# Optimization experiments

Hardware: AMD Instinct MI355X
Metric: run time of the kernel (lower is better)

Reference implementation:

```python
import jax, jax.numpy as jnp
import numpy as np

N_E = 1024
E_DIM = 64
BETA = 0.25
DECAY = 0.99
EPSILON = 1e-5


def setup_inputs() -> dict:
    key = jax.random.key(0)
    k1, k2, k3 = jax.random.split(key, 3)
    z = jax.random.normal(k1, (32, E_DIM, 32, 32), dtype=jnp.float32)
    # codebook initialized uniform(-1/n_e, 1/n_e) as in the torch module
    emb_w = jax.random.uniform(k2, (N_E, E_DIM), minval=-1.0 / N_E, maxval=1.0 / N_E, dtype=jnp.float32)
    ema_cluster_size = jnp.ones((N_E,), dtype=jnp.float32)
    ema_w = jax.random.uniform(k3, (N_E, E_DIM), minval=-1.0 / N_E, maxval=1.0 / N_E, dtype=jnp.float32)
    return {"z": z, "emb_w": emb_w, "ema_cluster_size": ema_cluster_size, "ema_w": ema_w}


def reference(z, emb_w, ema_cluster_size, ema_w):
    B, C, H, W = z.shape  # C == E_DIM
    zf = jnp.transpose(z, (0, 2, 3, 1)).reshape(-1, E_DIM)  # [N, e_dim]
    N = zf.shape[0]

    # squared-distance via ||z||^2 + ||e||^2 - 2 z.e (same expansion as torch code)
    d = (jnp.sum(zf * zf, axis=1, keepdims=True)
         + jnp.sum(emb_w * emb_w, axis=1)
         - 2.0 * zf @ emb_w.T)  # [N, n_e]
    idx = jnp.argmin(d, axis=1)  # [N]

    min_encodings = jax.nn.one_hot(idx, N_E, dtype=jnp.float32)  # [N, n_e]
    # cluster stats via scatter-add (equivalent to one-hot matmuls, cheaper)
    cluster_size = jax.ops.segment_sum(jnp.ones((N,), jnp.float32), idx, num_segments=N_E)
    sum_encodings = jax.ops.segment_sum(zf, idx, num_segments=N_E)  # [n_e, e_dim]

    # EMA update (training path, done before the z_q lookup as in torch)
    new_cs = DECAY * ema_cluster_size + (1.0 - DECAY) * cluster_size
    new_w = DECAY * ema_w + (1.0 - DECAY) * sum_encodings
    n = jnp.sum(new_cs)
    cs_norm = (new_cs + EPSILON) / (n + N_E * EPSILON) * n
    new_emb = new_w / cs_norm[:, None]  # updated codebook

    z_q = new_emb[idx].reshape(B, H, W, C).transpose(0, 3, 1, 2)  # [B,C,H,W]
    loss = BETA * jnp.mean((jax.lax.stop_gradient(z_q) - z) ** 2)
    z_q_st = z + jax.lax.stop_gradient(z_q - z)  # straight-through

    avg_probs = cluster_size / N
    perplexity = jnp.exp(-jnp.sum(avg_probs * jnp.log(avg_probs + 1e-10)))
    return loss, z_q_st, perplexity, min_encodings, idx
```

## Files before the change

kernel.cpp:

```cpp
#include <hip/hip_runtime.h>
#include <math.h>

#define NVEC 32768
#define NE   1024
#define ED   64
#define TOT  2097152
#define NCHUNK 4
#define CHUNK  256
#define MT     128

#define O_LOSS   0
#define O_ZQ     1
#define O_PERP   2097153
#define O_MINENC 2097154
#define O_IDX    35651586

#define W_PIDX   0
#define W_CS     32768
#define W_SUMENC 33792
#define W_ESQ    164864


__global__ void __launch_bounds__(256) k_pre(const float* __restrict__ emb,
                                             float* __restrict__ ws,
                                             float* __restrict__ out) {
    int b = blockIdx.x;
    if (b < 65) {
        int i = b * 256 + threadIdx.x;
        float4 zv; zv.x = 0.f; zv.y = 0.f; zv.z = 0.f; zv.w = 0.f;
        *(float4*)(ws + W_CS + i * 4) = zv;
        if (b == 0 && threadIdx.x == 0) out[O_LOSS] = 0.f;
    } else {
        int code = (b - 65) * 256 + threadIdx.x;
        const float* ep = emb + (size_t)code * ED;
        float r[8];
#pragma unroll
        for (int j = 0; j < 8; ++j) r[j] = __fmul_rn(ep[j], ep[j]);
#pragma unroll
        for (int i = 8; i < 64; i += 8)
#pragma unroll
            for (int j = 0; j < 8; ++j)
                r[j] = __fadd_rn(r[j], __fmul_rn(ep[i + j], ep[i + j]));
        ws[W_ESQ + code] = __fadd_rn(
            __fadd_rn(__fadd_rn(r[0], r[1]), __fadd_rn(r[2], r[3])),
            __fadd_rn(__fadd_rn(r[4], r[5]), __fadd_rn(r[6], r[7])));
    }
}

__device__ __forceinline__ int apos(int m) {
    return ((m & 4) << 4) + ((m >> 3) << 2) + (m & 3);
}

__global__ void __launch_bounds__(512) k_dist(const float* __restrict__ z,
                                              const float* __restrict__ emb,
                                              const float* __restrict__ esq_g,
                                              int* __restrict__ fidx,
                                              int* __restrict__ cnt,
                                              float* __restrict__ sumenc,
                                              float* __restrict__ out) {
    __shared__ __align__(16) float s_a[64 * 128];
    __shared__ __align__(16) float s_b[2 * 64 * 132];
    __shared__ float s_esq[CHUNK];
    __shared__ float s_zsq[MT];
    __shared__ int s_bi[MT];

    int tid = threadIdx.x;
    int n0 = blockIdx.x * MT;
    int b = n0 >> 10, hw0 = n0 & 1023;
    const float* zb = z + b * 65536 + hw0;

#pragma unroll
    for (int j = 0; j < 4; ++j) {
        int f4i = j * 512 + tid;
        int q = f4i & 31, c = f4i >> 5;
        float4 v = *(const float4*)(zb + (c << 10) + q * 4);
        v.x = __fmul_rn(2.0f, v.x);
        v.y = __fmul_rn(2.0f, v.y);
        v.z = __fmul_rn(2.0f, v.z);
        v.w = __fmul_rn(2.0f, v.w);
        *(float4*)(s_a + c * 128 + ((q & 1) << 6) + ((q >> 1) << 2)) = v;
    }
    __syncthreads();

    if (tid < MT) {
        int p = apos(tid);
        float r[8];
#pragma unroll
        for (int j = 0; j < 8; ++j) {
            float v = s_a[j * 128 + p];
            r[j] = __fmul_rn(v, v);
        }
#pragma unroll
        for (int i = 8; i < 64; i += 8)
#pragma unroll
            for (int j = 0; j < 8; ++j) {
                float v = s_a[(i + j) * 128 + p];
                r[j] = __fadd_rn(r[j], __fmul_rn(v, v));
            }
        s_zsq[tid] = __fmul_rn(0.25f, __fadd_rn(
            __fadd_rn(__fadd_rn(r[0], r[1]), __fadd_rn(r[2], r[3])),
            __fadd_rn(__fadd_rn(r[4], r[5]), __fadd_rn(r[6], r[7]))));
    }
    __syncthreads();

    int mi = tid & 15, ki = tid >> 4;
    int kbase = ki * 8;
    int kk = ki & 15;
    const float* sbk = s_b + (ki >> 4) * 8448;
    float zs[8];
#pragma unroll
    for (int mu = 0; mu < 8; ++mu) zs[mu] = s_zsq[8 * mi + mu];

    float bd[8];
    int bix[8];
#pragma unroll
    for (int mu = 0; mu < 8; ++mu) { bd[mu] = 3.4e38f; bix[mu] = kbase; }

    for (int ch = 0; ch < NCHUNK; ++ch) {
        int k0 = ch * CHUNK;
        __syncthreads();
#pragma unroll
        for (int j = 0; j < 8; ++j) {
            int f4i = j * 512 + tid;
            int kl = f4i >> 4, c4 = f4i & 15;
            float4 v = *(const float4*)(emb + (size_t)(k0 + kl) * ED + c4 * 4);
            int sc = kl >> 7, klr = kl & 127;
            float* sb = s_b + sc * 8448;
            int base = (((klr >> 2) + c4) & 31) * 4 + (klr & 3);
            sb[(c4 * 4 + 0) * 132 + base] = v.x;
            sb[(c4 * 4 + 1) * 132 + base] = v.y;
            sb[(c4 * 4 + 2) * 132 + base] = v.z;
            sb[(c4 * 4 + 3) * 132 + base] = v.w;
        }
        if (tid < CHUNK) s_esq[tid] = esq_g[k0 + tid];
        __syncthreads();

        float acc[8][8];
#pragma unroll
        for (int mu = 0; mu < 8; ++mu)
#pragma unroll
            for (int ku = 0; ku < 8; ++ku) acc[mu][ku] = 0.f;

        for (int cg = 0; cg < 64; cg += 4) {
            float4 A0[4], A1[4], B0[4], B1[4];
#pragma unroll
            for (int j = 0; j < 4; ++j) {
                int c = cg + j;
                int c4 = c >> 2;
                const float* ar = s_a + c * 128 + (mi << 2);
                A0[j] = *(const float4*)(ar);
                A1[j] = *(const float4*)(ar + 64);
                B0[j] = *(const float4*)(sbk + c * 132 + ((2 * kk + c4) & 31) * 4);
                B1[j] = *(const float4*)(sbk + c * 132 + ((2 * kk + 1 + c4) & 31) * 4);
            }
#pragma unroll
            for (int j = 0; j < 4; ++j) {
#pragma unroll
                for (int mu = 0; mu < 8; ++mu) {
                    float a = (mu < 4) ? (&A0[j].x)[mu] : (&A1[j].x)[mu - 4];
                    acc[mu][0] = __fmaf_rn(a, B0[j].x, acc[mu][0]);
                    acc[mu][1] = __fmaf_rn(a, B0[j].y, acc[mu][1]);
                    acc[mu][2] = __fmaf_rn(a, B0[j].z, acc[mu][2]);
                    acc[mu][3] = __fmaf_rn(a, B0[j].w, acc[mu][3]);
                    acc[mu][4] = __fmaf_rn(a, B1[j].x, acc[mu][4]);
                    acc[mu][5] = __fmaf_rn(a, B1[j].y, acc[mu][5]);
                    acc[mu][6] = __fmaf_rn(a, B1[j].z, acc[mu][6]);
                    acc[mu][7] = __fmaf_rn(a, B1[j].w, acc[mu][7]);
                }
            }
        }

#pragma unroll
        for (int mu = 0; mu < 8; ++mu)
#pragma unroll
            for (int ku = 0; ku < 8; ++ku) {
                float d = __fsub_rn(__fadd_rn(zs[mu], s_esq[kbase + ku]),
                                    acc[mu][ku]);
                if (d < bd[mu]) { bd[mu] = d; bix[mu] = k0 + kbase + ku; }
            }
    }

    __syncthreads();
    float* red_d = s_b;
    int* red_i = (int*)(s_b + 4096);
#pragma unroll
    for (int mu = 0; mu < 8; ++mu) {
        red_d[ki * 128 + 8 * mi + mu] = bd[mu];
        red_i[ki * 128 + 8 * mi + mu] = bix[mu];
    }
    __syncthreads();
    if (tid < MT) {
        float best = red_d[tid];
        int bi = red_i[tid];
#pragma unroll
        for (int q = 1; q < 32; ++q) {
            float d = red_d[q * 128 + tid];
            int i = red_i[q * 128 + tid];
            if (d < best || (d == best && i < bi)) { best = d; bi = i; }
        }
        fidx[n0 + tid] = bi;
        out[O_IDX + n0 + tid] = (float)bi;
        s_bi[tid] = bi;
        atomicAdd(&cnt[bi], 1);
    }
    __syncthreads();

    {
        int m = tid & 127, qt = tid >> 7;
        int p = apos(m);
#pragma unroll
        for (int j = 0; j < 16; ++j) {
            int c = qt * 16 + j;
            s_b[m * 65 + c] = __fmul_rn(0.5f, s_a[c * 128 + p]);
        }
    }
    __syncthreads();

    {
        int lane = tid & 63, w = tid >> 6;
#pragma unroll
        for (int t = 0; t < 16; ++t) {
            int m = (w << 4) | t;
            int bi = s_bi[m];
            float v = s_b[m * 65 + lane];
            unsafeAtomicAdd(sumenc + ((size_t)bi << 6) + lane, v);
        }
    }
}

__global__ void __launch_bounds__(256) k_zq(const float* __restrict__ z,
                                            const int* __restrict__ idx,
                                            const float* __restrict__ ema_cs,
                                            const float* __restrict__ ema_w,
                                            const int* __restrict__ cnt,
                                            const float* __restrict__ sumenc,
                                            float* __restrict__ out) {
    __shared__ float s_csn[NE];
    __shared__ float swn[4], swe[4];
    __shared__ int sbi[16];
    int tid = threadIdx.x;
    bool doent = (blockIdx.x == 0);

    float myncs[4];
    float rn = 0.f, re = 0.f;
#pragma unroll
    for (int j = 0; j < 4; ++j) {
        int k = j * 256 + tid;
        float c = (float)cnt[k];
        float ncs = 0.99f * ema_cs[k] + (1.0f - 0.99f) * c;
        myncs[j] = ncs;
        rn += ncs;
        if (doent) {
            float p = c * (1.0f / (float)NVEC);
            re += p * logf(p + 1e-10f);
        }
    }
#pragma unroll
    for (int o = 32; o > 0; o >>= 1) {
        rn += __shfl_down(rn, o, 64);
        re += __shfl_down(re, o, 64);
    }
    int wave = tid >> 6;
    if ((tid & 63) == 0) { swn[wave] = rn; swe[wave] = re; }
    if (tid < 16) sbi[tid] = idx[blockIdx.x * 16 + tid];
    __syncthreads();
    float nt = (swn[0] + swn[1]) + (swn[2] + swn[3]);
    if (doent && tid == 0) {
        float te = (swe[0] + swe[1]) + (swe[2] + swe[3]);
        out[O_PERP] = expf(-te);
    }
#pragma unroll
    for (int j = 0; j < 4; ++j) {
        int k = j * 256 + tid;
        s_csn[k] = (myncs[j] + 1e-5f) / (nt + 1024.0f * 1e-5f) * nt;
    }
    __syncthreads();

    float local = 0.f;
#pragma unroll
    for (int i = 0; i < 4; ++i) {
        int t = blockIdx.x * 256 + tid + i * 524288;
        int b = t >> 16, c = (t >> 10) & 63, hw = t & 1023;
        int n = (b << 10) | hw;
        int g = idx[n] * ED + c;
        float nw = 0.99f * ema_w[g] + (1.0f - 0.99f) * sumenc[g];
        float e = nw / s_csn[g >> 6];
        float zv = z[t];
        float diff = e - zv;
        out[O_ZQ + t] = zv + diff;
        local = fmaf(diff, diff, local);
    }

    int t = tid;
    int r0 = blockIdx.x * 16;
    for (int r = 0; r < 16; ++r) {
        int rbi = sbi[r];
        float* rp = out + O_MINENC + (size_t)(r0 + r) * NE;
        if (t < 254) {
            int col = 2 + t * 4;
            float4 v;
            v.x = (col == rbi) ? 1.0f : 0.0f;
            v.y = (col + 1 == rbi) ? 1.0f : 0.0f;
            v.z = (col + 2 == rbi) ? 1.0f : 0.0f;
            v.w = (col + 3 == rbi) ? 1.0f : 0.0f;
            *(float4*)(rp + col) = v;
        } else if (t == 254) {
            float2 v;
            v.x = (0 == rbi) ? 1.0f : 0.0f;
            v.y = (1 == rbi) ? 1.0f : 0.0f;
            *(float2*)(rp) = v;
        } else {
            float4 v;
            v.x = (1018 == rbi) ? 1.0f : 0.0f;
            v.y = (1019 == rbi) ? 1.0f : 0.0f;
            v.z = (1020 == rbi) ? 1.0f : 0.0f;
            v.w = (1021 == rbi) ? 1.0f : 0.0f;
            *(float4*)(rp + 1018) = v;
            float2 w;
            w.x = (1022 == rbi) ? 1.0f : 0.0f;
            w.y = (1023 == rbi) ? 1.0f : 0.0f;
            *(float2*)(rp + 1022) = w;
        }
    }

#pragma unroll
    for (int o = 32; o > 0; o >>= 1) local += __shfl_down(local, o, 64);
    __shared__ float sp[4];
    if ((tid & 63) == 0) sp[wave] = local;
    __syncthreads();
    if (tid == 0)
        unsafeAtomicAdd(out + O_LOSS,
                        ((sp[0] + sp[1]) + (sp[2] + sp[3])) * (0.25f / (float)TOT));
}

extern "C" void kernel_launch(void* const* d_in, const int* in_sizes, int n_in,
                              void* d_out, int out_size, void* d_ws, size_t ws_size,
                              hipStream_t stream) {
    const float* z      = (const float*)d_in[0];
    const float* emb    = (const float*)d_in[1];
    const float* ema_cs = (const float*)d_in[2];
    const float* ema_w  = (const float*)d_in[3];
    float* out = (float*)d_out;
    float* ws  = (float*)d_ws;

    k_pre<<<69, 256, 0, stream>>>(emb, ws, out);
    k_dist<<<NVEC / MT, 512, 0, stream>>>(z, emb, ws + W_ESQ, (int*)(ws + W_PIDX),
                                          (int*)(ws + W_CS), ws + W_SUMENC, out);
    k_zq<<<2048, 256, 0, stream>>>(z, (const int*)(ws + W_PIDX), ema_cs, ema_w,
                                   (const int*)(ws + W_CS), ws + W_SUMENC, out);
}
```

Baseline: 244.3 us.

## Read codebook directly from global/L1 instead of staging chunks in LDS

The distance kernel no longer copies 256-code chunks of the codebook into shared memory with block-wide barriers. Each thread now loads its own 8 codebook rows straight from global memory (through cache) as float4s, and all 1024 squared norms are preloaded once. This removes the per-chunk LDS transpose stores and syncs and shrinks shared memory use, which may raise occupancy. In exchange, codebook reads become per-thread strided global loads that rely on L1/L2 hit rates, and lanes in a wavefront read overlapping rows.

```diff
diff --git a/kernel.cpp b/kernel.cpp
--- a/kernel.cpp
+++ b/kernel.cpp
@@ -5,9 +5,7 @@
 #define NE   1024
 #define ED   64
 #define TOT  2097152
-#define NCHUNK 4
-#define CHUNK  256
-#define MT     128
+#define MT   128
 
 #define O_LOSS   0
 #define O_ZQ     1
@@ -59,8 +57,8 @@
                                               float* __restrict__ sumenc,
                                               float* __restrict__ out) {
     __shared__ __align__(16) float s_a[64 * 128];
-    __shared__ __align__(16) float s_b[2 * 64 * 132];
-    __shared__ float s_esq[CHUNK];
+    __shared__ __align__(16) float s_scr[8448];
+    __shared__ float s_esq[NE];
     __shared__ float s_zsq[MT];
     __shared__ int s_bi[MT];
 
@@ -80,6 +78,8 @@
         v.w = __fmul_rn(2.0f, v.w);
         *(float4*)(s_a + c * 128 + ((q & 1) << 6) + ((q >> 1) << 2)) = v;
     }
+    s_esq[tid] = esq_g[tid];
+    s_esq[tid + 512] = esq_g[tid + 512];
     __syncthreads();
 
     if (tid < MT) {
@@ -104,9 +104,7 @@
     __syncthreads();
 
     int mi = tid & 15, ki = tid >> 4;
-    int kbase = ki * 8;
-    int kk = ki & 15;
-    const float* sbk = s_b + (ki >> 4) * 8448;
+    int kb8 = ki * 8;
     float zs[8];
 #pragma unroll
     for (int mu = 0; mu < 8; ++mu) zs[mu] = s_zsq[8 * mi + mu];
@@ -114,26 +112,11 @@
     float bd[8];
     int bix[8];
 #pragma unroll
-    for (int mu = 0; mu < 8; ++mu) { bd[mu] = 3.4e38f; bix[mu] = kbase; }
-
-    for (int ch = 0; ch < NCHUNK; ++ch) {
-        int k0 = ch * CHUNK;
-        __syncthreads();
-#pragma unroll
-        for (int j = 0; j < 8; ++j) {
-            int f4i = j * 512 + tid;
-            int kl = f4i >> 4, c4 = f4i & 15;
-            float4 v = *(const float4*)(emb + (size_t)(k0 + kl) * ED + c4 * 4);
-            int sc = kl >> 7, klr = kl & 127;
-            float* sb = s_b + sc * 8448;
-            int base = (((klr >> 2) + c4) & 31) * 4 + (klr & 3);
-            sb[(c4 * 4 + 0) * 132 + base] = v.x;
-            sb[(c4 * 4 + 1) * 132 + base] = v.y;
-            sb[(c4 * 4 + 2) * 132 + base] = v.z;
-            sb[(c4 * 4 + 3) * 132 + base] = v.w;
-        }
-        if (tid < CHUNK) s_esq[tid] = esq_g[k0 + tid];
-        __syncthreads();
+    for (int mu = 0; mu < 8; ++mu) { bd[mu] = 3.4e38f; bix[mu] = kb8; }
+
+    for (int ch = 0; ch < 4; ++ch) {
+        int k0 = ch * 256;
+        const float* eb = emb + (size_t)(k0 + kb8) * ED;
 
         float acc[8][8];
 #pragma unroll
@@ -141,31 +124,24 @@
 #pragma unroll
             for (int ku = 0; ku < 8; ++ku) acc[mu][ku] = 0.f;
 
-        for (int cg = 0; cg < 64; cg += 4) {
-            float4 A0[4], A1[4], B0[4], B1[4];
+#pragma unroll 4
+        for (int c4 = 0; c4 < 16; ++c4) {
+            float4 B[8];
+#pragma unroll
+            for (int ku = 0; ku < 8; ++ku)
+                B[ku] = *(const float4*)(eb + ku * ED + c4 * 4);
 #pragma unroll
             for (int j = 0; j < 4; ++j) {
-                int c = cg + j;
-                int c4 = c >> 2;
+                int c = c4 * 4 + j;
                 const float* ar = s_a + c * 128 + (mi << 2);
-                A0[j] = *(const float4*)(ar);
-                A1[j] = *(const float4*)(ar + 64);
-                B0[j] = *(const float4*)(sbk + c * 132 + ((2 * kk + c4) & 31) * 4);
-                B1[j] = *(const float4*)(sbk + c * 132 + ((2 * kk + 1 + c4) & 31) * 4);
-            }
-#pragma unroll
-            for (int j = 0; j < 4; ++j) {
+                float4 a0 = *(const float4*)(ar);
+                float4 a1 = *(const float4*)(ar + 64);
 #pragma unroll
                 for (int mu = 0; mu < 8; ++mu) {
-                    float a = (mu < 4) ? (&A0[j].x)[mu] : (&A1[j].x)[mu - 4];
-                    acc[mu][0] = __fmaf_rn(a, B0[j].x, acc[mu][0]);
-                    acc[mu][1] = __fmaf_rn(a, B0[j].y, acc[mu][1]);
-                    acc[mu][2] = __fmaf_rn(a, B0[j].z, acc[mu][2]);
-                    acc[mu][3] = __fmaf_rn(a, B0[j].w, acc[mu][3]);
-                    acc[mu][4] = __fmaf_rn(a, B1[j].x, acc[mu][4]);
-                    acc[mu][5] = __fmaf_rn(a, B1[j].y, acc[mu][5]);
-                    acc[mu][6] = __fmaf_rn(a, B1[j].z, acc[mu][6]);
-                    acc[mu][7] = __fmaf_rn(a, B1[j].w, acc[mu][7]);
+                    float a = (mu < 4) ? (&a0.x)[mu] : (&a1.x)[mu - 4];
+#pragma unroll
+                    for (int ku = 0; ku < 8; ++ku)
+                        acc[mu][ku] = __fmaf_rn(a, (&B[ku].x)[j], acc[mu][ku]);
                 }
             }
         }
@@ -174,15 +150,14 @@
         for (int mu = 0; mu < 8; ++mu)
 #pragma unroll
             for (int ku = 0; ku < 8; ++ku) {
-                float d = __fsub_rn(__fadd_rn(zs[mu], s_esq[kbase + ku]),
+                float d = __fsub_rn(__fadd_rn(zs[mu], s_esq[k0 + kb8 + ku]),
                                     acc[mu][ku]);
-                if (d < bd[mu]) { bd[mu] = d; bix[mu] = k0 + kbase + ku; }
+                if (d < bd[mu]) { bd[mu] = d; bix[mu] = k0 + kb8 + ku; }
             }
     }
 
-    __syncthreads();
-    float* red_d = s_b;
-    int* red_i = (int*)(s_b + 4096);
+    float* red_d = s_scr;
+    int* red_i = (int*)(s_scr + 4096);
 #pragma unroll
     for (int mu = 0; mu < 8; ++mu) {
         red_d[ki * 128 + 8 * mi + mu] = bd[mu];
@@ -211,7 +186,7 @@
 #pragma unroll
         for (int j = 0; j < 16; ++j) {
             int c = qt * 16 + j;
-            s_b[m * 65 + c] = __fmul_rn(0.5f, s_a[c * 128 + p]);
+            s_scr[m * 65 + c] = __fmul_rn(0.5f, s_a[c * 128 + p]);
         }
     }
     __syncthreads();
@@ -222,7 +197,7 @@
         for (int t = 0; t < 16; ++t) {
             int m = (w << 4) | t;
             int bi = s_bi[m];
-            float v = s_b[m * 65 + lane];
+            float v = s_scr[m * 65 + lane];
             unsafeAtomicAdd(sumenc + ((size_t)bi << 6) + lane, v);
         }
     }
```

New measurement: 250.7 us. 2.6% more time.

## Split codebook search across two blocks per tile and add merge kernel

Applied to the files above, without the earlier changes.

The distance kernel now launches two 256-thread blocks per 128-vector tile. Each block scans half the codebook and writes its partial best distance and index into scratch space in the min_encodings output region. A new merge kernel picks the winner, writes the indices and counts, and does the sum-of-encodings atomics by reading z directly. The aim is more blocks and smaller LDS use per block, for better occupancy. The cost is an extra kernel launch and extra global traffic, and the scratch use of the output buffer relies on k_zq overwriting min_encodings later.

```diff
diff --git a/kernel.cpp b/kernel.cpp
--- a/kernel.cpp
+++ b/kernel.cpp
@@ -6,7 +6,7 @@
 #define ED   64
 #define TOT  2097152
 #define NCHUNK 4
-#define CHUNK  256
+#define CHUNK  128
 #define MT     128
 
 #define O_LOSS   0
@@ -51,27 +51,24 @@
     return ((m & 4) << 4) + ((m >> 3) << 2) + (m & 3);
 }
 
-__global__ void __launch_bounds__(512) k_dist(const float* __restrict__ z,
+__global__ void __launch_bounds__(256) k_dist(const float* __restrict__ z,
                                               const float* __restrict__ emb,
                                               const float* __restrict__ esq_g,
-                                              int* __restrict__ fidx,
-                                              int* __restrict__ cnt,
-                                              float* __restrict__ sumenc,
                                               float* __restrict__ out) {
     __shared__ __align__(16) float s_a[64 * 128];
-    __shared__ __align__(16) float s_b[2 * 64 * 132];
+    __shared__ __align__(16) float s_b[64 * 132];
     __shared__ float s_esq[CHUNK];
     __shared__ float s_zsq[MT];
-    __shared__ int s_bi[MT];
 
     int tid = threadIdx.x;
-    int n0 = blockIdx.x * MT;
+    int tile = blockIdx.x >> 1, khalf = blockIdx.x & 1;
+    int n0 = tile * MT;
     int b = n0 >> 10, hw0 = n0 & 1023;
     const float* zb = z + b * 65536 + hw0;
 
 #pragma unroll
-    for (int j = 0; j < 4; ++j) {
-        int f4i = j * 512 + tid;
+    for (int j = 0; j < 8; ++j) {
+        int f4i = j * 256 + tid;
         int q = f4i & 31, c = f4i >> 5;
         float4 v = *(const float4*)(zb + (c << 10) + q * 4);
         v.x = __fmul_rn(2.0f, v.x);
@@ -105,8 +102,6 @@
 
     int mi = tid & 15, ki = tid >> 4;
     int kbase = ki * 8;
-    int kk = ki & 15;
-    const float* sbk = s_b + (ki >> 4) * 8448;
     float zs[8];
 #pragma unroll
     for (int mu = 0; mu < 8; ++mu) zs[mu] = s_zsq[8 * mi + mu];
@@ -114,23 +109,21 @@
     float bd[8];
     int bix[8];
 #pragma unroll
-    for (int mu = 0; mu < 8; ++mu) { bd[mu] = 3.4e38f; bix[mu] = kbase; }
+    for (int mu = 0; mu < 8; ++mu) { bd[mu] = 3.4e38f; bix[mu] = khalf * 512 + kbase; }
 
     for (int ch = 0; ch < NCHUNK; ++ch) {
-        int k0 = ch * CHUNK;
+        int k0 = khalf * 512 + ch * CHUNK;
         __syncthreads();
 #pragma unroll
         for (int j = 0; j < 8; ++j) {
-            int f4i = j * 512 + tid;
+            int f4i = j * 256 + tid;
             int kl = f4i >> 4, c4 = f4i & 15;
             float4 v = *(const float4*)(emb + (size_t)(k0 + kl) * ED + c4 * 4);
-            int sc = kl >> 7, klr = kl & 127;
-            float* sb = s_b + sc * 8448;
-            int base = (((klr >> 2) + c4) & 31) * 4 + (klr & 3);
-            sb[(c4 * 4 + 0) * 132 + base] = v.x;
-            sb[(c4 * 4 + 1) * 132 + base] = v.y;
-            sb[(c4 * 4 + 2) * 132 + base] = v.z;
-            sb[(c4 * 4 + 3) * 132 + base] = v.w;
+            int base = (((kl >> 2) + c4) & 31) * 4 + (kl & 3);
+            s_b[(c4 * 4 + 0) * 132 + base] = v.x;
+            s_b[(c4 * 4 + 1) * 132 + base] = v.y;
+            s_b[(c4 * 4 + 2) * 132 + base] = v.z;
+            s_b[(c4 * 4 + 3) * 132 + base] = v.w;
         }
         if (tid < CHUNK) s_esq[tid] = esq_g[k0 + tid];
         __syncthreads();
@@ -150,8 +143,8 @@
                 const float* ar = s_a + c * 128 + (mi << 2);
                 A0[j] = *(const float4*)(ar);
                 A1[j] = *(const float4*)(ar + 64);
-                B0[j] = *(const float4*)(sbk + c * 132 + ((2 * kk + c4) & 31) * 4);
-                B1[j] = *(const float4*)(sbk + c * 132 + ((2 * kk + 1 + c4) & 31) * 4);
+                B0[j] = *(const float4*)(s_b + c * 132 + ((2 * ki + c4) & 31) * 4);
+                B1[j] = *(const float4*)(s_b + c * 132 + ((2 * ki + 1 + c4) & 31) * 4);
             }
 #pragma unroll
             for (int j = 0; j < 4; ++j) {
@@ -182,7 +175,7 @@
 
     __syncthreads();
     float* red_d = s_b;
-    int* red_i = (int*)(s_b + 4096);
+    int* red_i = (int*)(s_b + 2048);
 #pragma unroll
     for (int mu = 0; mu < 8; ++mu) {
         red_d[ki * 128 + 8 * mi + mu] = bd[mu];
@@ -193,37 +186,54 @@
         float best = red_d[tid];
         int bi = red_i[tid];
 #pragma unroll
-        for (int q = 1; q < 32; ++q) {
+        for (int q = 1; q < 16; ++q) {
             float d = red_d[q * 128 + tid];
             int i = red_i[q * 128 + tid];
             if (d < best || (d == best && i < bi)) { best = d; bi = i; }
         }
-        fidx[n0 + tid] = bi;
-        out[O_IDX + n0 + tid] = (float)bi;
+        out[O_MINENC + khalf * 32768 + n0 + tid] = best;
+        ((int*)(out + O_MINENC))[65536 + khalf * 32768 + n0 + tid] = bi;
+    }
+}
+
+__global__ void __launch_bounds__(256) k_mrg(const float* __restrict__ z,
+                                             int* __restrict__ fidx,
+                                             int* __restrict__ cnt,
+                                             float* __restrict__ sumenc,
+                                             float* __restrict__ out) {
+    __shared__ int s_bi[MT];
+    int tid = threadIdx.x;
+    int m0 = blockIdx.x * MT;
+
+    if (tid < MT) {
+        int m = m0 + tid;
+        const float* cd = out + O_MINENC;
+        const int* ci = (const int*)(out + O_MINENC) + 65536;
+        float d0 = cd[m], d1 = cd[32768 + m];
+        int i0 = ci[m], i1 = ci[32768 + m];
+        int bi = (d1 < d0) ? i1 : i0;
+        fidx[m] = bi;
+        out[O_IDX + m] = (float)bi;
         s_bi[tid] = bi;
         atomicAdd(&cnt[bi], 1);
     }
     __syncthreads();
 
-    {
-        int m = tid & 127, qt = tid >> 7;
-        int p = apos(m);
-#pragma unroll
-        for (int j = 0; j < 16; ++j) {
-            int c = qt * 16 + j;
-            s_b[m * 65 + c] = __fmul_rn(0.5f, s_a[c * 128 + p]);
-        }
-    }
-    __syncthreads();
-
-    {
-        int lane = tid & 63, w = tid >> 6;
-#pragma unroll
-        for (int t = 0; t < 16; ++t) {
-            int m = (w << 4) | t;
-            int bi = s_bi[m];
-            float v = s_b[m * 65 + lane];
-            unsafeAtomicAdd(sumenc + ((size_t)bi << 6) + lane, v);
+    int lane = tid & 63, w = tid >> 6;
+    int b = m0 >> 10, hw0 = m0 & 1023;
+    const float* zc = z + b * 65536 + lane * 1024 + hw0;
+#pragma unroll
+    for (int t0 = 0; t0 < 32; t0 += 4) {
+        float v[4];
+#pragma unroll
+        for (int u = 0; u < 4; ++u) {
+            int ml = (w << 5) + t0 + u;
+            v[u] = zc[ml];
+        }
+#pragma unroll
+        for (int u = 0; u < 4; ++u) {
+            int ml = (w << 5) + t0 + u;
+            unsafeAtomicAdd(sumenc + ((size_t)s_bi[ml] << 6) + lane, v[u]);
         }
     }
 }
@@ -344,8 +354,9 @@
     float* ws  = (float*)d_ws;
 
     k_pre<<<69, 256, 0, stream>>>(emb, ws, out);
-    k_dist<<<NVEC / MT, 512, 0, stream>>>(z, emb, ws + W_ESQ, (int*)(ws + W_PIDX),
-                                          (int*)(ws + W_CS), ws + W_SUMENC, out);
+    k_dist<<<512, 256, 0, stream>>>(z, emb, ws + W_ESQ, out);
+    k_mrg<<<256, 256, 0, stream>>>(z, (int*)(ws + W_PIDX), (int*)(ws + W_CS),
+                                   ws + W_SUMENC, out);
     k_zq<<<2048, 256, 0, stream>>>(z, (const int*)(ws + W_PIDX), ema_cs, ema_w,
                                    (const int*)(ws + W_CS), ws + W_SUMENC, out);
 }
```

Measured after the change: 246.0 us. About the same (+0.7%).
